# Optimization experiments

Hardware: AMD Instinct MI355X
Metric: run time of the kernel (lower is better)

Reference implementation:

```python
import jax, jax.numpy as jnp
import numpy as np

N_NODES = 50000
N_EDGES = 800000
D_IN = 128
D_OUT = 128


def setup_inputs() -> dict:
    key = jax.random.key(0)
    k1, k2, k3, k4, k5, k6 = jax.random.split(key, 6)
    feat = jax.random.normal(k1, (N_NODES, D_IN), dtype=jnp.float32)
    src = jax.random.randint(k2, (N_EDGES,), 0, N_NODES, dtype=jnp.int64)
    dst = jax.random.randint(k3, (N_EDGES,), 0, N_NODES, dtype=jnp.int64)
    # Glorot-like scale for the linear weights (fc_neigh has no bias; fc_self has bias)
    scale = 1.0 / np.sqrt(D_IN)
    W_neigh = jax.random.normal(k4, (D_OUT, D_IN), dtype=jnp.float32) * scale
    W_self = jax.random.normal(k5, (D_OUT, D_IN), dtype=jnp.float32) * scale
    b_self = jax.random.normal(k6, (D_OUT,), dtype=jnp.float32) * scale
    return {"feat": feat, "src": src, "dst": dst,
            "W_neigh": W_neigh, "W_self": W_self, "b_self": b_self}


def reference(feat, src, dst, W_neigh, W_self, b_self):
    """SAGEConv with aggregator_type='mean', feat_drop=0, bias=True.

    in_feats == out_feats (128) -> lin_before_mp is False:
      h_neigh = fc_neigh(mean over incoming neighbors of feat)
      out     = fc_self(feat) + h_neigh
    """
    n = feat.shape[0]
    # message passing: copy_u + fn.mean('m', 'neigh')
    msgs = feat[src]                                            # [E, D_in]
    summed = jax.ops.segment_sum(msgs, dst, num_segments=n)     # [N, D_in]
    deg = jax.ops.segment_sum(jnp.ones((src.shape[0],), feat.dtype),
                              dst, num_segments=n)              # [N]
    # zero in-degree -> neigh = 0 (matches DGL mean semantics)
    h_neigh = summed / jnp.maximum(deg, 1.0)[:, None]
    h_neigh = h_neigh @ W_neigh.T                               # fc_neigh (no bias)
    h_self = feat @ W_self.T + b_self                           # fc_self (bias)
    return h_self + h_neigh
```

## Files before the change

### kernel.cpp

```cpp
#include <hip/hip_runtime.h>
#include <hip/hip_bf16.h>

typedef __hip_bfloat16 bf16;
typedef __attribute__((ext_vector_type(8))) short bf16x8;
typedef __attribute__((ext_vector_type(4))) float f32x4;
#define DIM 128
#define BK 64
#define PCAP 4096
#define CHUNK 4096
#define EPT 16

__device__ __forceinline__ float bfbits(unsigned short u) {
    return __uint_as_float(((unsigned)u) << 16);
}
__device__ __forceinline__ unsigned short f2bf(float f) {
    bf16 h = __float2bfloat16(f);
    return *(unsigned short*)&h;
}
__device__ __forceinline__ void load8(const void* p, int is32, size_t off, float* f) {
    if (is32) {
        const float* q = (const float*)p + off;
        float4 a = *(const float4*)q;
        float4 b = *(const float4*)(q + 4);
        f[0] = a.x; f[1] = a.y; f[2] = a.z; f[3] = a.w;
        f[4] = b.x; f[5] = b.y; f[6] = b.z; f[7] = b.w;
    } else {
        uint4 v = *(const uint4*)((const unsigned short*)p + off);
        const unsigned int* w = (const unsigned int*)&v;
#pragma unroll
        for (int i = 0; i < 4; i++) {
            f[2 * i]     = __uint_as_float(w[i] << 16);
            f[2 * i + 1] = __uint_as_float(w[i] & 0xffff0000u);
        }
    }
}
__device__ __forceinline__ int read_idx(const void* p, int is64, int e) {
    return is64 ? (int)((const long long*)p)[e] : ((const int*)p)[e];
}

__device__ __forceinline__ int is_fp32_wave(const unsigned int* p, int lane) {
    unsigned w = p[lane];
    unsigned low = w & 0xFFFFu;
    unsigned ex = (low >> 7) & 0xFFu;
    bool hit = (ex >= 90u && ex <= 140u) || low == 0u || low == 0x8000u;
    unsigned long long m = __ballot(hit);
    return (2 * __popcll(m) < 64) ? 1 : 0;
}
__global__ void init_kernel(const unsigned int* __restrict__ src,
                            const unsigned int* __restrict__ feat,
                            const unsigned int* __restrict__ wn,
                            const unsigned int* __restrict__ wsm,
                            const unsigned int* __restrict__ bias,
                            int* __restrict__ flags, int* __restrict__ cnt, int Z) {
    int i = blockIdx.x * blockDim.x + threadIdx.x;
    if (i < Z) cnt[i] = 0;
    if (blockIdx.x == 0 && threadIdx.x < 64) {
        int lane = threadIdx.x;
        unsigned long long m = __ballot(src[1 + 2 * lane] != 0u);
        int f1 = is_fp32_wave(feat, lane);
        int f2 = is_fp32_wave(wn, lane);
        int f3 = is_fp32_wave(wsm, lane);
        int f4 = is_fp32_wave(bias, lane);
        if (lane == 0) {
            flags[0] = (m == 0ull) ? 1 : 0;
            flags[1] = f1; flags[2] = f2; flags[3] = f3; flags[4] = f4;
        }
    }
}

__global__ __launch_bounds__(256) void part_kernel(
    const void* __restrict__ srcv, const void* __restrict__ dstv,
    const int* __restrict__ flags, int* __restrict__ gcnt,
    unsigned* __restrict__ pbuf,
    const float* __restrict__ featf, unsigned short* __restrict__ wsbf,
    int E, int N, int eblocks, int total8, int nparts, int cstride) {
    __shared__ int hist[1024];
    __shared__ int bstart[1024];
    __shared__ int gbase[1024];
    __shared__ int tsum[256];
    __shared__ unsigned stage[CHUNK];

    int b = blockIdx.x;
    int t = threadIdx.x;

    if (b >= eblocks) {
        if (!flags[1]) return;
        for (int i = (b - eblocks) * 256 + t; i < total8; i += cstride) {
            size_t e = (size_t)i * 8;
            float4 a = *(const float4*)(featf + e);
            float4 bb = *(const float4*)(featf + e + 4);
            unsigned short u[8] = {f2bf(a.x), f2bf(a.y), f2bf(a.z), f2bf(a.w),
                                   f2bf(bb.x), f2bf(bb.y), f2bf(bb.z), f2bf(bb.w)};
            *(uint4*)(wsbf + e) = *(uint4*)u;
        }
        return;
    }

    int is64 = flags[0];
    for (int i = t; i < nparts; i += 256) hist[i] = 0;
    __syncthreads();

    unsigned v[EPT];
    int base = b * CHUNK;
#pragma unroll
    for (int j = 0; j < EPT; j++) {
        int e = base + j * 256 + t;
        unsigned val = 0xFFFFFFFFu;
        if (e < E) {
            int s = read_idx(srcv, is64, e);
            int d = read_idx(dstv, is64, e);
            if ((unsigned)s < (unsigned)N && (unsigned)d < (unsigned)N)
                val = ((unsigned)d << 16) | (unsigned)s;
        }
        v[j] = val;
        if (val != 0xFFFFFFFFu) atomicAdd(&hist[val >> 22], 1);
    }
    __syncthreads();

    int K = (nparts + 255) >> 8;
    int s0 = 0;
    for (int j = 0; j < K; j++) {
        int bin = t * K + j;
        if (bin < nparts) s0 += hist[bin];
    }
    tsum[t] = s0;
    __syncthreads();
    for (int off = 1; off < 256; off <<= 1) {
        int x = (t >= off) ? tsum[t - off] : 0;
        __syncthreads();
        tsum[t] += x;
        __syncthreads();
    }
    int tot = tsum[255];
    int run = (t > 0) ? tsum[t - 1] : 0;
    for (int j = 0; j < K; j++) {
        int bin = t * K + j;
        if (bin < nparts) {
            bstart[bin] = run;
            int h = hist[bin];
            run += h;
            gbase[bin] = h ? atomicAdd(&gcnt[bin], h) : 0;
        }
    }
    __syncthreads();
    for (int i = t; i < nparts; i += 256) hist[i] = bstart[i];
    __syncthreads();

#pragma unroll
    for (int j = 0; j < EPT; j++) {
        unsigned val = v[j];
        if (val != 0xFFFFFFFFu) {
            int bin = val >> 22;
            int p = atomicAdd(&hist[bin], 1);
            stage[p] = val;
        }
    }
    __syncthreads();

    for (int p = t; p < tot; p += 256) {
        unsigned val = stage[p];
        int bin = val >> 22;
        unsigned off = (unsigned)(gbase[bin] + (p - bstart[bin]));
        if (off < PCAP) pbuf[(size_t)bin * PCAP + off] = val;
    }
}

__global__ __launch_bounds__(256) void fused_kernel(
    const void* __restrict__ feat, const unsigned short* __restrict__ wsbf,
    const unsigned* __restrict__ pbuf, const int* __restrict__ gcnt,
    void* __restrict__ dout, int N, const int* __restrict__ flags) {
    __shared__ int cnt[64];
    __shared__ unsigned short list[64][64];

    int t = threadIdx.x;
    int p = blockIdx.x;
    int nbase = p << 6;
    int feat32 = flags[1];
    const unsigned short* sb = feat32 ? wsbf : (const unsigned short*)feat;

    if (t < 64) cnt[t] = 0;
    __syncthreads();

    int ec = gcnt[p];
    if (ec > PCAP) ec = PCAP;
    for (int i = t; i < ec; i += 256) {
        unsigned val = pbuf[(size_t)p * PCAP + i];
        int local = (int)(val >> 16) - nbase;
        int pos = atomicAdd(&cnt[local], 1);
        if (pos < 64) list[local][pos] = (unsigned short)(val & 0xFFFFu);
    }
    __syncthreads();

    int lane = t & 63;
    int wv = t >> 6;
    int grp = lane >> 4;
    int li = lane & 15;

    for (int q = 0; q < 16; q++) {
        int local = wv * 16 + q;
        int node = nbase + local;
        if (node >= N) break;
        int deg = cnt[local];
        int use = deg < 64 ? deg : 64;

        float acc[8];
#pragma unroll
        for (int i = 0; i < 8; i++) acc[i] = 0.f;

        for (int k = 0; k < use; k += 16) {
            uint4 v[4];
            float wgt[4];
#pragma unroll
            for (int j = 0; j < 4; j++) {
                int r = k + j * 4 + grp;
                wgt[j] = (r < use) ? 1.0f : 0.0f;
                int rc = (r < use) ? r : (use - 1);
                int s = list[local][rc];
                v[j] = *(const uint4*)(sb + (size_t)s * DIM + li * 8);
            }
#pragma unroll
            for (int j = 0; j < 4; j++) {
                const unsigned* w = (const unsigned*)&v[j];
#pragma unroll
                for (int i = 0; i < 4; i++) {
                    acc[2 * i]     = fmaf(wgt[j], __uint_as_float(w[i] << 16), acc[2 * i]);
                    acc[2 * i + 1] = fmaf(wgt[j], __uint_as_float(w[i] & 0xffff0000u), acc[2 * i + 1]);
                }
            }
        }

#pragma unroll
        for (int i = 0; i < 8; i++) {
            acc[i] += __shfl_xor(acc[i], 16);
            acc[i] += __shfl_xor(acc[i], 32);
        }

        float rd = 1.0f / fmaxf((float)deg, 1.0f);
        if (grp == 0) {
            unsigned short u[8];
#pragma unroll
            for (int i = 0; i < 8; i++) u[i] = f2bf(acc[i] * rd);
            size_t ob = feat32 ? ((size_t)node * 512 + 256 + (size_t)li * 16)
                               : ((size_t)node * 256 + (size_t)li * 16);
            *(uint4*)((char*)dout + ob) = *(uint4*)u;
        }
    }
}

__global__ void buckcvt_kernel(const void* __restrict__ srcv, const void* __restrict__ dstv,
                               const int* __restrict__ flags, int* __restrict__ cnt,
                               unsigned short* __restrict__ b16, int* __restrict__ b32,
                               const float* __restrict__ featf,
                               unsigned short* __restrict__ wsbf,
                               int E, int N, int eblocks, int total8, int use16, int ws_ok) {
    int b = blockIdx.x;
    if (b < eblocks) {
        int e = b * 256 + threadIdx.x;
        if (e >= E) return;
        int is64 = flags[0];
        int s = read_idx(srcv, is64, e);
        int d = read_idx(dstv, is64, e);
        if ((unsigned)s >= (unsigned)N || (unsigned)d >= (unsigned)N) return;
        int pos = atomicAdd(&cnt[d], 1);
        if (pos < BK) {
            if (use16) b16[(size_t)d * BK + pos] = (unsigned short)s;
            else       b32[(size_t)d * BK + pos] = s;
        }
    } else {
        if (!flags[1] || !ws_ok) return;
        int i = (b - eblocks) * 256 + threadIdx.x;
        if (i >= total8) return;
        size_t e = (size_t)i * 8;
        float4 a = *(const float4*)(featf + e);
        float4 bb = *(const float4*)(featf + e + 4);
        unsigned short u[8] = {f2bf(a.x), f2bf(a.y), f2bf(a.z), f2bf(a.w),
                               f2bf(bb.x), f2bf(bb.y), f2bf(bb.z), f2bf(bb.w)};
        *(uint4*)(wsbf + e) = *(uint4*)u;
    }
}

__global__ __launch_bounds__(256) void gather_kernel(
    const void* __restrict__ feat, const unsigned short* __restrict__ wsbf,
    const unsigned short* __restrict__ b16, const int* __restrict__ b32,
    const int* __restrict__ cnt, void* __restrict__ dout,
    int N, const int* __restrict__ flags, int use16, int ws_ok) {
    int t = threadIdx.x;
    int lane = t & 63;
    int wv = t >> 6;
    int node = blockIdx.x * 4 + wv;
    if (node >= N) return;
    int feat32 = flags[1];
    int bfmode = (!feat32) || ws_ok;
    const unsigned short* sb = feat32 ? wsbf : (const unsigned short*)feat;
    const float* ff = (const float*)feat;

    int deg = __builtin_amdgcn_readfirstlane(cnt[node]);
    int use = deg < BK ? deg : BK;
    int idxv;
    if (use16) idxv = b16[(size_t)node * BK + (lane < use ? lane : 0)];
    else       idxv = b32[(size_t)node * BK + (lane < use ? lane : 0)];

    float a0 = 0.f, a1 = 0.f;
    int k = 0;
    if (bfmode) {
        for (; k + 8 <= use; k += 8) {
            int ss[8];
#pragma unroll
            for (int j = 0; j < 8; j++) ss[j] = __shfl(idxv, k + j);
            unsigned uu[8];
#pragma unroll
            for (int j = 0; j < 8; j++)
                uu[j] = *(const unsigned*)(sb + (size_t)ss[j] * DIM + lane * 2);
#pragma unroll
            for (int j = 0; j < 8; j++) {
                a0 += bfbits((unsigned short)uu[j]);
                a1 += bfbits((unsigned short)(uu[j] >> 16));
            }
        }
        for (; k < use; k++) {
            int s = __shfl(idxv, k);
            unsigned u = *(const unsigned*)(sb + (size_t)s * DIM + lane * 2);
            a0 += bfbits((unsigned short)u);
            a1 += bfbits((unsigned short)(u >> 16));
        }
    } else {
        for (; k + 4 <= use; k += 4) {
            int s0 = __shfl(idxv, k),     s1 = __shfl(idxv, k + 1);
            int s2 = __shfl(idxv, k + 2), s3 = __shfl(idxv, k + 3);
            float2 v0 = *(const float2*)(ff + (size_t)s0 * DIM + lane * 2);
            float2 v1 = *(const float2*)(ff + (size_t)s1 * DIM + lane * 2);
            float2 v2 = *(const float2*)(ff + (size_t)s2 * DIM + lane * 2);
            float2 v3 = *(const float2*)(ff + (size_t)s3 * DIM + lane * 2);
            a0 += (v0.x + v1.x) + (v2.x + v3.x);
            a1 += (v0.y + v1.y) + (v2.y + v3.y);
        }
        for (; k < use; k++) {
            int s = __shfl(idxv, k);
            float2 v = *(const float2*)(ff + (size_t)s * DIM + lane * 2);
            a0 += v.x; a1 += v.y;
        }
    }

    float rd = 1.0f / fmaxf((float)deg, 1.0f);
    unsigned up = ((unsigned)f2bf(a1 * rd) << 16) | (unsigned)f2bf(a0 * rd);
    size_t ob = feat32 ? ((size_t)node * 512 + 256 + (size_t)lane * 4)
                       : ((size_t)node * 256 + (size_t)lane * 4);
    *(unsigned*)((char*)dout + ob) = up;
}

#define TPW 2
__global__ __launch_bounds__(256) void gemm_kernel(
    const void* __restrict__ feat, const unsigned short* __restrict__ wsbf,
    const void* __restrict__ Wn, const void* __restrict__ Ws,
    const void* __restrict__ bias, void* __restrict__ out,
    int N, const int* __restrict__ flags, int ws_ok) {
    __shared__ short ldsb[4096 * 8];

    int t = threadIdx.x;
    int lane = t & 63;
    int wv = t >> 6;
    int feat32 = flags[1], wn32 = flags[2], ws32 = flags[3], bs32 = flags[4];
    int bfmode = (!feat32) || ws_ok;

    for (int f = t; f < 4096; f += 256) {
        int tj = f >> 9, ks = (f >> 6) & 7, ln = f & 63;
        int j = tj * 16 + (ln & 15);
        int kk = ks * 32 + (ln >> 4) * 8;
        float w[8];
        if (kk < DIM) load8(Ws, ws32, (size_t)j * DIM + kk, w);
        else          load8(Wn, wn32, (size_t)j * DIM + (kk - DIM), w);
        unsigned short u[8];
#pragma unroll
        for (int i = 0; i < 8; i++) u[i] = f2bf(w[i]);
        *(uint4*)(ldsb + (size_t)f * 8) = *(uint4*)u;
    }
    __syncthreads();

    const bf16x8* bfrag = (const bf16x8*)ldsb;

    float bcol[8];
#pragma unroll
    for (int tj = 0; tj < 8; tj++) {
        int col = tj * 16 + (lane & 15);
        bcol[tj] = bs32 ? ((const float*)bias)[col]
                        : bfbits(((const unsigned short*)bias)[col]);
    }

    int quad = lane >> 4;
    int NT = (N + 15) >> 4;
    int gw = blockIdx.x * 4 + wv;

    const unsigned short* sb = feat32 ? wsbf : (const unsigned short*)feat;
    const char* hbase = (const char*)out;
    size_t hrow = feat32 ? 512 : 256;
    size_t hoff = feat32 ? 256 : 0;

    for (int it = 0; it < TPW; it++) {
        int tile = gw * TPW + it;
        if (tile >= NT) break;
        int tb = tile * 16;

        int arow = tb + (lane & 15);
        if (arow >= N) arow = N - 1;
        bf16x8 afr[8];
#pragma unroll
        for (int ks = 0; ks < 4; ks++) {
            int kk = ks * 32 + quad * 8;
            if (bfmode) {
                afr[ks] = *(const bf16x8*)(sb + (size_t)arow * DIM + kk);
            } else {
                float av[8];
                load8(feat, 1, (size_t)arow * DIM + kk, av);
                unsigned short u[8];
#pragma unroll
                for (int i = 0; i < 8; i++) u[i] = f2bf(av[i]);
                afr[ks] = *(bf16x8*)u;
            }
        }
#pragma unroll
        for (int ks = 4; ks < 8; ks++) {
            int kk = (ks - 4) * 32 + quad * 8;
            afr[ks] = *(const bf16x8*)(hbase + (size_t)arow * hrow + hoff + (size_t)kk * 2);
        }

        f32x4 acc[8];
#pragma unroll
        for (int tj = 0; tj < 8; tj++)
            acc[tj] = (f32x4){bcol[tj], bcol[tj], bcol[tj], bcol[tj]};

#pragma unroll
        for (int tj = 0; tj < 8; tj++) {
#pragma unroll
            for (int ks = 0; ks < 8; ks++) {
                acc[tj] = __builtin_amdgcn_mfma_f32_16x16x32_bf16(
                    afr[ks], bfrag[(tj * 8 + ks) * 64 + lane], acc[tj], 0, 0, 0);
            }
        }

#pragma unroll
        for (int tj = 0; tj < 8; tj++) {
            int col = tj * 16 + (lane & 15);
#pragma unroll
            for (int r = 0; r < 4; r++) {
                int row = tb + quad * 4 + r;
                if (row < N) {
                    size_t idx = (size_t)row * DIM + col;
                    if (feat32) ((float*)out)[idx] = acc[tj][r];
                    else ((unsigned short*)out)[idx] = f2bf(acc[tj][r]);
                }
            }
        }
    }
}

extern "C" void kernel_launch(void* const* d_in, const int* in_sizes, int n_in,
                              void* d_out, int out_size, void* d_ws, size_t ws_size,
                              hipStream_t stream) {
    const void* feat = d_in[0];
    const void* src  = d_in[1];
    const void* dst  = d_in[2];
    const void* Wn   = d_in[3];
    const void* Ws   = d_in[4];
    const void* bias = d_in[5];

    const int N = in_sizes[0] / DIM;
    const int E = in_sizes[1];
    const int use16 = (N <= 65535) ? 1 : 0;
    const int total8 = N * DIM / 8;
    int* flags = (int*)d_ws;

    const int nparts = (N + 63) >> 6;
    size_t pbuf_off = (64 + (size_t)nparts * 4 + 255) & ~(size_t)255;
    size_t wsf_off  = (pbuf_off + (size_t)nparts * PCAP * 4 + 255) & ~(size_t)255;
    size_t need_f   = wsf_off + (size_t)N * DIM * 2;
    const int FAST = (use16 && nparts <= 1024 && ws_size >= need_f) ? 1 : 0;

    if (FAST) {
        int* gcnt = (int*)((char*)d_ws + 64);
        unsigned* pbuf = (unsigned*)((char*)d_ws + pbuf_off);
        unsigned short* wsbf = (unsigned short*)((char*)d_ws + wsf_off);

        init_kernel<<<(nparts + 255) / 256, 256, 0, stream>>>(
            (const unsigned int*)src, (const unsigned int*)feat, (const unsigned int*)Wn,
            (const unsigned int*)Ws, (const unsigned int*)bias, flags, gcnt, nparts);

        int eb = (E + CHUNK - 1) / CHUNK;
        int cb = (total8 + 255) / 256;
        if (cb > 1024) cb = 1024;
        part_kernel<<<eb + cb, 256, 0, stream>>>(
            src, dst, flags, gcnt, pbuf, (const float*)feat, wsbf,
            E, N, eb, total8, nparts, cb * 256);

        fused_kernel<<<nparts, 256, 0, stream>>>(
            feat, wsbf, pbuf, gcnt, d_out, N, flags);

        int NT = (N + 15) / 16;
        int gwaves = (NT + TPW - 1) / TPW;
        gemm_kernel<<<(gwaves + 3) / 4, 256, 0, stream>>>(
            feat, wsbf, Wn, Ws, bias, d_out, N, flags, 1);
        return;
    }

    const size_t esz = use16 ? 2 : 4;
    int* cnt = flags + 16;
    unsigned short* b16 = (unsigned short*)(cnt + N);
    int* b32 = (int*)(cnt + N);
    size_t bucket_bytes = (size_t)N * BK * esz;
    size_t bf_off = (64 + (size_t)N * 4 + bucket_bytes + 15) & ~(size_t)15;
    unsigned short* wsbf = (unsigned short*)((char*)d_ws + bf_off);
    size_t need = bf_off + (size_t)N * DIM * 2;
    int ws_ok = (ws_size >= need) ? 1 : 0;

    init_kernel<<<(N + 255) / 256, 256, 0, stream>>>(
        (const unsigned int*)src, (const unsigned int*)feat, (const unsigned int*)Wn,
        (const unsigned int*)Ws, (const unsigned int*)bias, flags, cnt, N);

    int eblocks = (E + 255) / 256;
    int cblocks = ws_ok ? (total8 + 255) / 256 : 0;
    buckcvt_kernel<<<eblocks + cblocks, 256, 0, stream>>>(
        src, dst, flags, cnt, b16, b32, (const float*)feat, wsbf,
        E, N, eblocks, total8, use16, ws_ok);

    gather_kernel<<<(N + 3) / 4, 256, 0, stream>>>(
        feat, wsbf, b16, b32, cnt, d_out, N, flags, use16, ws_ok);

    int NT = (N + 15) / 16;
    int gwaves = (NT + TPW - 1) / TPW;
    gemm_kernel<<<(gwaves + 3) / 4, 256, 0, stream>>>(
        feat, wsbf, Wn, Ws, bias, d_out, N, flags, ws_ok);
}
```

Measured before the change: 160.9 us.

## Split neighbor aggregation across four blocks per partition and interleave two GEMM tiles

The fused aggregation kernel now launches four blocks per 64-node partition. Each block filters the partition's edge list down to its own 16 nodes, so each wave processes 4 nodes instead of 16 and more blocks run in parallel. The cost is that every partition's edge buffer is read four times. The GEMM kernel drops its per-wave tile loop and computes two 16-row tiles at once, interleaving their MFMA chains so each B fragment load is shared and more independent work is in flight. That rewrite assumes TPW equals 2 and uses more registers.

```diff
diff --git a/kernel.cpp b/kernel.cpp
--- a/kernel.cpp
+++ b/kernel.cpp
@@ -169,16 +169,17 @@
     const void* __restrict__ feat, const unsigned short* __restrict__ wsbf,
     const unsigned* __restrict__ pbuf, const int* __restrict__ gcnt,
     void* __restrict__ dout, int N, const int* __restrict__ flags) {
-    __shared__ int cnt[64];
-    __shared__ unsigned short list[64][64];
+    __shared__ int cnt[16];
+    __shared__ unsigned short list[16][64];
 
     int t = threadIdx.x;
-    int p = blockIdx.x;
+    int p = blockIdx.x >> 2;
+    int qq = blockIdx.x & 3;
     int nbase = p << 6;
     int feat32 = flags[1];
     const unsigned short* sb = feat32 ? wsbf : (const unsigned short*)feat;
 
-    if (t < 64) cnt[t] = 0;
+    if (t < 16) cnt[t] = 0;
     __syncthreads();
 
     int ec = gcnt[p];
@@ -186,8 +187,10 @@
     for (int i = t; i < ec; i += 256) {
         unsigned val = pbuf[(size_t)p * PCAP + i];
         int local = (int)(val >> 16) - nbase;
-        int pos = atomicAdd(&cnt[local], 1);
-        if (pos < 64) list[local][pos] = (unsigned short)(val & 0xFFFFu);
+        if ((local >> 4) == qq) {
+            int pos = atomicAdd(&cnt[local & 15], 1);
+            if (pos < 64) list[local & 15][pos] = (unsigned short)(val & 0xFFFFu);
+        }
     }
     __syncthreads();
 
@@ -196,11 +199,11 @@
     int grp = lane >> 4;
     int li = lane & 15;
 
-    for (int q = 0; q < 16; q++) {
-        int local = wv * 16 + q;
-        int node = nbase + local;
+    for (int q = 0; q < 4; q++) {
+        int l16 = wv * 4 + q;
+        int node = nbase + (qq << 4) + l16;
         if (node >= N) break;
-        int deg = cnt[local];
+        int deg = cnt[l16];
         int use = deg < 64 ? deg : 64;
 
         float acc[8];
@@ -215,7 +218,7 @@
                 int r = k + j * 4 + grp;
                 wgt[j] = (r < use) ? 1.0f : 0.0f;
                 int rc = (r < use) ? r : (use - 1);
-                int s = list[local][rc];
+                int s = list[l16][rc];
                 v[j] = *(const uint4*)(sb + (size_t)s * DIM + li * 8);
             }
 #pragma unroll
@@ -395,58 +398,76 @@
     size_t hrow = feat32 ? 512 : 256;
     size_t hoff = feat32 ? 256 : 0;
 
-    for (int it = 0; it < TPW; it++) {
-        int tile = gw * TPW + it;
-        if (tile >= NT) break;
-        int tb = tile * 16;
-
-        int arow = tb + (lane & 15);
-        if (arow >= N) arow = N - 1;
-        bf16x8 afr[8];
-#pragma unroll
-        for (int ks = 0; ks < 4; ks++) {
-            int kk = ks * 32 + quad * 8;
-            if (bfmode) {
-                afr[ks] = *(const bf16x8*)(sb + (size_t)arow * DIM + kk);
-            } else {
-                float av[8];
-                load8(feat, 1, (size_t)arow * DIM + kk, av);
-                unsigned short u[8];
-#pragma unroll
-                for (int i = 0; i < 8; i++) u[i] = f2bf(av[i]);
-                afr[ks] = *(bf16x8*)u;
+    int tile0 = gw * TPW;
+    int tile1 = tile0 + 1;
+    if (tile0 >= NT) return;
+    int has1 = (tile1 < NT);
+    int tb0 = tile0 * 16;
+    int tb1 = has1 ? tile1 * 16 : tb0;
+
+    int arow0 = tb0 + (lane & 15); if (arow0 >= N) arow0 = N - 1;
+    int arow1 = tb1 + (lane & 15); if (arow1 >= N) arow1 = N - 1;
+
+    bf16x8 afr0[8], afr1[8];
+#pragma unroll
+    for (int ks = 0; ks < 4; ks++) {
+        int kk = ks * 32 + quad * 8;
+        if (bfmode) {
+            afr0[ks] = *(const bf16x8*)(sb + (size_t)arow0 * DIM + kk);
+            afr1[ks] = *(const bf16x8*)(sb + (size_t)arow1 * DIM + kk);
+        } else {
+            float av[8]; unsigned short u[8];
+            load8(feat, 1, (size_t)arow0 * DIM + kk, av);
+#pragma unroll
+            for (int i = 0; i < 8; i++) u[i] = f2bf(av[i]);
+            afr0[ks] = *(bf16x8*)u;
+            load8(feat, 1, (size_t)arow1 * DIM + kk, av);
+#pragma unroll
+            for (int i = 0; i < 8; i++) u[i] = f2bf(av[i]);
+            afr1[ks] = *(bf16x8*)u;
+        }
+    }
+#pragma unroll
+    for (int ks = 4; ks < 8; ks++) {
+        int kk = (ks - 4) * 32 + quad * 8;
+        afr0[ks] = *(const bf16x8*)(hbase + (size_t)arow0 * hrow + hoff + (size_t)kk * 2);
+        afr1[ks] = *(const bf16x8*)(hbase + (size_t)arow1 * hrow + hoff + (size_t)kk * 2);
+    }
+
+    f32x4 acc0[8], acc1[8];
+#pragma unroll
+    for (int tj = 0; tj < 8; tj++) {
+        acc0[tj] = (f32x4){bcol[tj], bcol[tj], bcol[tj], bcol[tj]};
+        acc1[tj] = acc0[tj];
+    }
+
+#pragma unroll
+    for (int tj = 0; tj < 8; tj++) {
+#pragma unroll
+        for (int ks = 0; ks < 8; ks++) {
+            bf16x8 bf = bfrag[(tj * 8 + ks) * 64 + lane];
+            acc0[tj] = __builtin_amdgcn_mfma_f32_16x16x32_bf16(afr0[ks], bf, acc0[tj], 0, 0, 0);
+            acc1[tj] = __builtin_amdgcn_mfma_f32_16x16x32_bf16(afr1[ks], bf, acc1[tj], 0, 0, 0);
+        }
+    }
+
+#pragma unroll
+    for (int tj = 0; tj < 8; tj++) {
+        int col = tj * 16 + (lane & 15);
+#pragma unroll
+        for (int r = 0; r < 4; r++) {
+            int row0 = tb0 + quad * 4 + r;
+            if (row0 < N) {
+                size_t idx = (size_t)row0 * DIM + col;
+                if (feat32) ((float*)out)[idx] = acc0[tj][r];
+                else ((unsigned short*)out)[idx] = f2bf(acc0[tj][r]);
             }
-        }
-#pragma unroll
-        for (int ks = 4; ks < 8; ks++) {
-            int kk = (ks - 4) * 32 + quad * 8;
-            afr[ks] = *(const bf16x8*)(hbase + (size_t)arow * hrow + hoff + (size_t)kk * 2);
-        }
-
-        f32x4 acc[8];
-#pragma unroll
-        for (int tj = 0; tj < 8; tj++)
-            acc[tj] = (f32x4){bcol[tj], bcol[tj], bcol[tj], bcol[tj]};
-
-#pragma unroll
-        for (int tj = 0; tj < 8; tj++) {
-#pragma unroll
-            for (int ks = 0; ks < 8; ks++) {
-                acc[tj] = __builtin_amdgcn_mfma_f32_16x16x32_bf16(
-                    afr[ks], bfrag[(tj * 8 + ks) * 64 + lane], acc[tj], 0, 0, 0);
-            }
-        }
-
-#pragma unroll
-        for (int tj = 0; tj < 8; tj++) {
-            int col = tj * 16 + (lane & 15);
-#pragma unroll
-            for (int r = 0; r < 4; r++) {
-                int row = tb + quad * 4 + r;
-                if (row < N) {
-                    size_t idx = (size_t)row * DIM + col;
-                    if (feat32) ((float*)out)[idx] = acc[tj][r];
-                    else ((unsigned short*)out)[idx] = f2bf(acc[tj][r]);
+            if (has1) {
+                int row1 = tb1 + quad * 4 + r;
+                if (row1 < N) {
+                    size_t idx = (size_t)row1 * DIM + col;
+                    if (feat32) ((float*)out)[idx] = acc1[tj][r];
+                    else ((unsigned short*)out)[idx] = f2bf(acc1[tj][r]);
                 }
             }
         }
@@ -491,7 +512,7 @@
             src, dst, flags, gcnt, pbuf, (const float*)feat, wsbf,
             E, N, eb, total8, nparts, cb * 256);
 
-        fused_kernel<<<nparts, 256, 0, stream>>>(
+        fused_kernel<<<nparts * 4, 256, 0, stream>>>(
             feat, wsbf, pbuf, gcnt, d_out, N, flags);
 
         int NT = (N + 15) / 16;
```

Measured after the change: 160.0 us. Within noise of the previous version (-0.6%).
